# Optimization experiments

Measured on AMD Instinct MI355X. Metric: run time of the kernel, lower is better.

Reference implementation:

```python
import jax, jax.numpy as jnp
import numpy as np

N, E, D, H = 100000, 1000000, 64, 4
HD = D // H  # head dim
G = 64       # num graphs in batch
EPS = 1e-5
NEG_SLOPE = 0.2


def setup_inputs() -> dict:
    key = jax.random.key(0)
    ks = jax.random.split(key, 10)
    x = jax.random.normal(ks[0], (N, D), dtype=jnp.float32)
    edge_index = jax.random.randint(ks[1], (2, E), 0, N)
    batch = jnp.sort(jax.random.randint(ks[2], (N,), 0, G))
    s = 1.0 / np.sqrt(D)
    Wl = jax.random.uniform(ks[3], (D, D), jnp.float32, -s, s)   # lin_l (source)
    Wr = jax.random.uniform(ks[4], (D, D), jnp.float32, -s, s)   # lin_r (target)
    att = jax.random.uniform(ks[5], (H, HD), jnp.float32, -s, s)
    bias_gat = jnp.zeros((D,), jnp.float32)
    gn_weight = jnp.ones((D,), jnp.float32)
    gn_bias = jnp.zeros((D,), jnp.float32)
    gn_mean_scale = jnp.ones((D,), jnp.float32)
    return {"x": x, "edge_index": edge_index, "batch": batch, "Wl": Wl,
            "Wr": Wr, "att": att, "bias_gat": bias_gat, "gn_weight": gn_weight,
            "gn_bias": gn_bias, "gn_mean_scale": gn_mean_scale}


def _gatv2(x, src, dst, Wl, Wr, att, bias_gat):
    # per-node linear projections, reshaped to heads
    xl = (x @ Wl).reshape(N, H, HD)  # source features
    xr = (x @ Wr).reshape(N, H, HD)  # target features
    # per-edge attention logits: a^T LeakyReLU(xl_j + xr_i)
    e = xl[src] + xr[dst]                             # [E', H, HD]
    e = jnp.where(e >= 0, e, NEG_SLOPE * e)           # leaky_relu
    score = jnp.einsum('ehd,hd->eh', e, att)          # [E', H]
    # segment softmax over incoming edges of each dst node
    m = jax.ops.segment_max(score, dst, num_segments=N)   # [N, H]
    p = jnp.exp(score - m[dst])
    denom = jax.ops.segment_sum(p, dst, num_segments=N)   # [N, H]
    alpha = p / denom[dst]                                # [E', H]
    # weighted scatter-add aggregation of source features
    out = jax.ops.segment_sum(alpha[:, :, None] * xl[src], dst, num_segments=N)
    return out.reshape(N, D) + bias_gat


def _graph_norm(h, batch, weight, bias, mean_scale):
    cnt = jax.ops.segment_sum(jnp.ones((N,), h.dtype), batch, num_segments=G)
    cnt = jnp.maximum(cnt, 1.0)[:, None]                      # [G,1]
    mean = jax.ops.segment_sum(h, batch, num_segments=G) / cnt
    out = h - mean_scale * mean[batch]
    var = jax.ops.segment_sum(out * out, batch, num_segments=G) / cnt
    return weight * out / jnp.sqrt(var[batch] + EPS) + bias


def reference(x, edge_index, batch, Wl, Wr, att, bias_gat, gn_weight, gn_bias, gn_mean_scale):
    # eval mode: dropout / DropEdge are identity; pre_norm=False; res_proj=Identity
    loops = jnp.arange(N)
    src = jnp.concatenate([edge_index[0], loops])  # add self-loops (PyG default)
    dst = jnp.concatenate([edge_index[1], loops])
    h = _gatv2(x, src, dst, Wl, Wr, att, bias_gat)
    h = h + x                                       # identity residual
    h = jnp.where(h > 0, h, jnp.expm1(h))           # ELU
    h = _graph_norm(h, batch, gn_weight, gn_bias, gn_mean_scale)
    return h
```

## Files before the change

### kernel.cpp

```cpp
#include <hip/hip_runtime.h>
#include <hip/hip_bf16.h>
#include <math.h>

#define G_ 64
#define NEG_SLOPE 0.2f
#define EPS_ 1e-5f
#define BBITS 7
#define BSZ 128
#define CAP 2048
#define EPB 4096

typedef __attribute__((ext_vector_type(8))) unsigned short ushort8;
typedef __attribute__((ext_vector_type(8))) short bf16x8;
typedef __attribute__((ext_vector_type(4))) float f32x4;

#define DPP_ADD(t, ctrl)                                                   \
  do {                                                                     \
    int _p = __builtin_amdgcn_update_dpp(0, __float_as_int(t), (ctrl),     \
                                         0xf, 0xf, true);                  \
    (t) += __int_as_float(_p);                                             \
  } while (0)
#define REDUCE16(t)                                                        \
  do {                                                                     \
    DPP_ADD(t, 0xB1);                                                      \
    DPP_ADD(t, 0x4E);                                                      \
    DPP_ADD(t, 0x141);                                                     \
    DPP_ADD(t, 0x140);                                                     \
  } while (0)

__device__ __forceinline__ float leaky_(float e) {
  return 0.6f * e + 0.4f * fabsf(e);
}

__device__ __forceinline__ short f2bf(float f) {
  __hip_bfloat16 h = __float2bfloat16(f);
  return *reinterpret_cast<short*>(&h);
}

__global__ __launch_bounds__(256) void proj_mfma_kernel(
    const float* __restrict__ x, const float* __restrict__ Wl,
    const float* __restrict__ Wr, __hip_bfloat16* __restrict__ xlb,
    __hip_bfloat16* __restrict__ xrb, int n) {
  const int lane = threadIdx.x & 63;
  const int wv = threadIdx.x >> 6;
  const int rbase = blockIdx.x * 64 + wv * 16;
  const int lrow = lane & 15;
  const int lgrp = lane >> 4;

  bf16x8 bfrag[8][2];
#pragma unroll
  for (int ct = 0; ct < 8; ++ct) {
    const float* W = (ct < 4) ? Wl : Wr;
    const int col = ((ct & 3) * 16) + lrow;
#pragma unroll
    for (int kk = 0; kk < 2; ++kk) {
      const int kb = kk * 32 + lgrp * 8;
      bf16x8 f;
#pragma unroll
      for (int j = 0; j < 8; ++j) f[j] = f2bf(W[(kb + j) * 64 + col]);
      bfrag[ct][kk] = f;
    }
  }

  bf16x8 afrag[2];
  const int r = rbase + lrow;
#pragma unroll
  for (int kk = 0; kk < 2; ++kk) {
    bf16x8 f;
    if (r < n) {
      const float4* p = (const float4*)(x + (size_t)r * 64 + kk * 32 + lgrp * 8);
      float4 u = p[0], v = p[1];
      f[0] = f2bf(u.x); f[1] = f2bf(u.y); f[2] = f2bf(u.z); f[3] = f2bf(u.w);
      f[4] = f2bf(v.x); f[5] = f2bf(v.y); f[6] = f2bf(v.z); f[7] = f2bf(v.w);
    } else {
      f = bf16x8{0, 0, 0, 0, 0, 0, 0, 0};
    }
    afrag[kk] = f;
  }

  f32x4 acc[8];
#pragma unroll
  for (int ct = 0; ct < 8; ++ct) acc[ct] = f32x4{0.f, 0.f, 0.f, 0.f};
#pragma unroll
  for (int ct = 0; ct < 8; ++ct)
#pragma unroll
    for (int kk = 0; kk < 2; ++kk)
      acc[ct] = __builtin_amdgcn_mfma_f32_16x16x32_bf16(
          afrag[kk], bfrag[ct][kk], acc[ct], 0, 0, 0);

#pragma unroll
  for (int ct = 0; ct < 8; ++ct) {
    __hip_bfloat16* dst = (ct < 4) ? xlb : xrb;
    const int c = ((ct & 3) * 16) + lrow;
#pragma unroll
    for (int j = 0; j < 4; ++j) {
      const int rr = rbase + lgrp * 4 + j;
      if (rr < n) dst[(size_t)rr * 64 + c] = __float2bfloat16(acc[ct][j]);
    }
  }
}

__global__ __launch_bounds__(256) void bucket_kernel(
    const int* __restrict__ esrc, const int* __restrict__ edst,
    int* __restrict__ bcnt, unsigned int* __restrict__ packed,
    int e, int nb) {
  __shared__ int cnt[800];
  __shared__ int base[800];
  const int t = threadIdx.x;
  const int e0 = blockIdx.x * EPB;
  const int e1 = (e0 + EPB) < e ? (e0 + EPB) : e;
  for (int b = t; b < nb; b += 256) cnt[b] = 0;
  __syncthreads();
  for (int i = e0 + t; i < e1; i += 256)
    atomicAdd(&cnt[edst[i] >> BBITS], 1);
  __syncthreads();
  for (int b = t; b < nb; b += 256) {
    int c = cnt[b];
    base[b] = c ? atomicAdd(&bcnt[b], c) : 0;
    cnt[b] = 0;
  }
  __syncthreads();
  for (int i = e0 + t; i < e1; i += 256) {
    int d = edst[i];
    int b = d >> BBITS;
    int pos = base[b] + atomicAdd(&cnt[b], 1);
    if (pos < CAP)
      packed[(size_t)b * CAP + pos] =
          ((unsigned)(d & (BSZ - 1)) << 17) | (unsigned)esrc[i];
  }
}

__global__ __launch_bounds__(256) void sort_kernel(
    unsigned int* __restrict__ packed, const int* __restrict__ bcnt,
    int2* __restrict__ nse, int n) {
  __shared__ unsigned int stage[CAP];
  __shared__ int cnt[BSZ];
  __shared__ int sc[BSZ];
  __shared__ int off[BSZ + 1];
  const int t = threadIdx.x;
  const int b = blockIdx.x;
  int ecnt = bcnt[b];
  if (ecnt > CAP) ecnt = CAP;
  for (int j = t; j < ecnt; j += 256) stage[j] = packed[(size_t)b * CAP + j];
  if (t < BSZ) cnt[t] = 0;
  __syncthreads();
  for (int j = t; j < ecnt; j += 256) atomicAdd(&cnt[stage[j] >> 17], 1);
  __syncthreads();
  if (t < BSZ) sc[t] = cnt[t];
  __syncthreads();
#pragma unroll
  for (int o = 1; o < BSZ; o <<= 1) {
    int v = 0;
    if (t < BSZ && t >= o) v = sc[t - o];
    __syncthreads();
    if (t < BSZ) sc[t] += v;
    __syncthreads();
  }
  if (t < BSZ) {
    off[t + 1] = sc[t];
    if (t == 0) off[0] = 0;
    cnt[t] = sc[t] - cnt[t];
  }
  __syncthreads();
  for (int j = t; j < ecnt; j += 256) {
    unsigned v = stage[j];
    int pos = atomicAdd(&cnt[v >> 17], 1);
    packed[(size_t)b * CAP + pos] = v & 0x1FFFF;
  }
  const int nodebase = b << BBITS;
  if (t < BSZ && nodebase + t < n) {
    int s = off[t];
    nse[nodebase + t] = make_int2(b * CAP + s, off[t + 1] - s);
  }
}

__global__ __launch_bounds__(256) void aggregate_kernel(
    const __hip_bfloat16* __restrict__ xlb,
    const __hip_bfloat16* __restrict__ xrb, const float* __restrict__ x,
    const float* __restrict__ att, const float* __restrict__ bias_gat,
    const int2* __restrict__ nse, const unsigned int* __restrict__ srt,
    __hip_bfloat16* __restrict__ hb, int n) {
  const int lane = threadIdx.x & 63;
  const int i = (blockIdx.x * blockDim.x + threadIdx.x) >> 6;
  if (i >= n) return;
  const float attv = att[lane];
  const size_t rowoff = (size_t)i * 64 + lane;
  const float xrv = __bfloat162float(xrb[rowoff]);
  const float xlv = __bfloat162float(xlb[rowoff]);
  float t0 = leaky_(xlv + xrv) * attv;
  REDUCE16(t0);
  float p0 = __expf(t0);
  float acc = p0 * xlv;
  float den = p0;
  int2 sd = nse[i];
  const int s0 = __builtin_amdgcn_readfirstlane(sd.x);
  const int deg = __builtin_amdgcn_readfirstlane(sd.y);
  int myedge = (lane < deg) ? (int)srt[s0 + lane] : 0;
  const int kmax = deg < 64 ? deg : 64;
  int k = 0;
  for (; k + 3 < kmax; k += 4) {
    int sa = __builtin_amdgcn_readlane(myedge, k);
    int sb = __builtin_amdgcn_readlane(myedge, k + 1);
    int sc = __builtin_amdgcn_readlane(myedge, k + 2);
    int sdl = __builtin_amdgcn_readlane(myedge, k + 3);
    float xa = __bfloat162float(xlb[(size_t)sa * 64 + lane]);
    float xb = __bfloat162float(xlb[(size_t)sb * 64 + lane]);
    float xc = __bfloat162float(xlb[(size_t)sc * 64 + lane]);
    float xd = __bfloat162float(xlb[(size_t)sdl * 64 + lane]);
    float ta = leaky_(xa + xrv) * attv;
    float tb = leaky_(xb + xrv) * attv;
    float tc = leaky_(xc + xrv) * attv;
    float td = leaky_(xd + xrv) * attv;
    DPP_ADD(ta, 0xB1); DPP_ADD(tb, 0xB1); DPP_ADD(tc, 0xB1); DPP_ADD(td, 0xB1);
    DPP_ADD(ta, 0x4E); DPP_ADD(tb, 0x4E); DPP_ADD(tc, 0x4E); DPP_ADD(td, 0x4E);
    DPP_ADD(ta, 0x141); DPP_ADD(tb, 0x141); DPP_ADD(tc, 0x141); DPP_ADD(td, 0x141);
    DPP_ADD(ta, 0x140); DPP_ADD(tb, 0x140); DPP_ADD(tc, 0x140); DPP_ADD(td, 0x140);
    float pa = __expf(ta), pb = __expf(tb), pc = __expf(tc), pd = __expf(td);
    acc += pa * xa + pb * xb;
    acc += pc * xc + pd * xd;
    den += (pa + pb) + (pc + pd);
  }
  for (; k < kmax; ++k) {
    int s = __builtin_amdgcn_readlane(myedge, k);
    float xs = __bfloat162float(xlb[(size_t)s * 64 + lane]);
    float tt = leaky_(xs + xrv) * attv;
    REDUCE16(tt);
    float pp = __expf(tt);
    acc += pp * xs;
    den += pp;
  }
  for (int kk = 64; kk < deg; ++kk) {
    int s = (int)srt[s0 + kk];
    float xs = __bfloat162float(xlb[(size_t)s * 64 + lane]);
    float tt = leaky_(xs + xrv) * attv;
    REDUCE16(tt);
    float pp = __expf(tt);
    acc += pp * xs;
    den += pp;
  }
  float hv = acc / den + bias_gat[lane] + x[rowoff];
  hv = hv > 0.f ? hv : expm1f(hv);
  hb[rowoff] = __float2bfloat16(hv);
}

__global__ __launch_bounds__(256) void gsum2_kernel(
    const __hip_bfloat16* __restrict__ h, const int* __restrict__ batch,
    float* __restrict__ gsum, float* __restrict__ gsq,
    float* __restrict__ gcnt, int n) {
  const int lane = threadIdx.x & 63;
  const int wave = (blockIdx.x * blockDim.x + threadIdx.x) >> 6;
  const int nwaves = (gridDim.x * blockDim.x) >> 6;
  const int chunk = (n + nwaves - 1) / nwaves;
  const int start = wave * chunk;
  const int end = (start + chunk) < n ? (start + chunk) : n;
  float s1 = 0.f, s2 = 0.f, cntl = 0.f;
  int curg = -1;
  for (int i = start; i < end; ++i) {
    int g = batch[i];
    if (g != curg) {
      if (curg >= 0) {
        atomicAdd(&gsum[curg * 64 + lane], s1);
        atomicAdd(&gsq[curg * 64 + lane], s2);
        if (lane == 0) atomicAdd(&gcnt[curg], cntl);
      }
      curg = g; s1 = 0.f; s2 = 0.f; cntl = 0.f;
    }
    float hv = __bfloat162float(h[(size_t)i * 64 + lane]);
    s1 += hv;
    s2 += hv * hv;
    cntl += 1.f;
  }
  if (curg >= 0) {
    atomicAdd(&gsum[curg * 64 + lane], s1);
    atomicAdd(&gsq[curg * 64 + lane], s2);
    if (lane == 0) atomicAdd(&gcnt[curg], cntl);
  }
}

__global__ void stats_kernel(const float* __restrict__ gsum,
                             const float* __restrict__ gsq,
                             const float* __restrict__ gcnt,
                             const float* __restrict__ mscale,
                             const float* __restrict__ w,
                             float* __restrict__ msmean,
                             float* __restrict__ scale) {
  int i = blockIdx.x * blockDim.x + threadIdx.x;
  if (i < G_ * 64) {
    int dd = i & 63;
    float c = gcnt[i >> 6];
    c = c > 1.f ? c : 1.f;
    float mean = gsum[i] / c;
    float ms = mscale[dd];
    float var = gsq[i] / c - ms * (2.f - ms) * mean * mean;
    msmean[i] = ms * mean;
    scale[i] = w[dd] * rsqrtf(var + EPS_);
  }
}

__global__ __launch_bounds__(256) void out_kernel(
    const __hip_bfloat16* __restrict__ hb, const int* __restrict__ batch,
    const float* __restrict__ msmean, const float* __restrict__ scale,
    const float* __restrict__ bias, float* __restrict__ out, int n) {
  const int total8 = n * 8;
  for (int idx = blockIdx.x * blockDim.x + threadIdx.x; idx < total8;
       idx += gridDim.x * blockDim.x) {
    int i = idx >> 3, q = idx & 7;
    int g = batch[i];
    int base = g * 64 + q * 8;
    ushort8 hv8 = ((const ushort8*)hb)[idx];
    float r[8];
#pragma unroll
    for (int j = 0; j < 8; ++j) {
      float f = __uint_as_float(((unsigned)hv8[j]) << 16);
      r[j] = (f - msmean[base + j]) * scale[base + j] + bias[q * 8 + j];
    }
    float4 o0 = make_float4(r[0], r[1], r[2], r[3]);
    float4 o1 = make_float4(r[4], r[5], r[6], r[7]);
    ((float4*)out)[idx * 2] = o0;
    ((float4*)out)[idx * 2 + 1] = o1;
  }
}

extern "C" void kernel_launch(void* const* d_in, const int* in_sizes, int n_in,
                              void* d_out, int out_size, void* d_ws, size_t ws_size,
                              hipStream_t stream) {
  const float* x        = (const float*)d_in[0];
  const int*   eidx     = (const int*)d_in[1];
  const int*   batch    = (const int*)d_in[2];
  const float* Wl       = (const float*)d_in[3];
  const float* Wr       = (const float*)d_in[4];
  const float* att      = (const float*)d_in[5];
  const float* bias_gat = (const float*)d_in[6];
  const float* gw       = (const float*)d_in[7];
  const float* gb       = (const float*)d_in[8];
  const float* gms      = (const float*)d_in[9];
  const int N = in_sizes[0] / 64;
  const int E = in_sizes[1] / 2;
  const int* esrc = eidx;
  const int* edst = eidx + E;
  float* out = (float*)d_out;
  const int NB = (N + BSZ - 1) >> BBITS;

  char* wsp = (char*)d_ws;
  float* gsum   = (float*)wsp;                wsp += G_ * 64 * 4;
  float* gsq    = (float*)wsp;                wsp += G_ * 64 * 4;
  float* gcnt   = (float*)wsp;                wsp += G_ * 4;
  float* msmean = (float*)wsp;                wsp += G_ * 64 * 4;
  float* scale  = (float*)wsp;                wsp += G_ * 64 * 4;
  int*   bcnt   = (int*)wsp;                  wsp += (size_t)NB * 4;
  int2*  nse    = (int2*)wsp;                 wsp += (size_t)N * 8;
  unsigned int* packed = (unsigned int*)wsp;  wsp += (size_t)NB * CAP * 4;
  __hip_bfloat16* xlb = (__hip_bfloat16*)wsp; wsp += (size_t)N * 64 * 2;
  __hip_bfloat16* xrb = (__hip_bfloat16*)wsp; wsp += (size_t)N * 64 * 2;
  __hip_bfloat16* hb  = (__hip_bfloat16*)wsp; wsp += (size_t)N * 64 * 2;

  hipMemsetAsync(gsum, 0, (size_t)(2 * G_ * 64 + G_) * sizeof(float), stream);
  hipMemsetAsync(bcnt, 0, (size_t)NB * sizeof(int), stream);

  proj_mfma_kernel<<<(N + 63) / 64, 256, 0, stream>>>(x, Wl, Wr, xlb, xrb, N);

  const int ab = (E + EPB - 1) / EPB;
  bucket_kernel<<<ab, 256, 0, stream>>>(esrc, edst, bcnt, packed, E, NB);
  sort_kernel<<<NB, 256, 0, stream>>>(packed, bcnt, nse, N);

  aggregate_kernel<<<(N + 3) / 4, 256, 0, stream>>>(
      xlb, xrb, x, att, bias_gat, nse, packed, hb, N);

  gsum2_kernel<<<1024, 256, 0, stream>>>(hb, batch, gsum, gsq, gcnt, N);
  stats_kernel<<<(G_ * 64 + 255) / 256, 256, 0, stream>>>(gsum, gsq, gcnt, gms,
                                                          gw, msmean, scale);
  out_kernel<<<3125, 256, 0, stream>>>(hb, batch, msmean, scale, gb, out, N);
}
```

Baseline: 166.6 us.

## Process two edges per wave with half-wave lanes handling packed bf16 pairs

New measurement: 178.4 us. 7.1% more time.

```diff
diff --git a/kernel.cpp b/kernel.cpp
--- a/kernel.cpp
+++ b/kernel.cpp
@@ -8,7 +8,7 @@
 #define BBITS 7
 #define BSZ 128
 #define CAP 2048
-#define EPB 4096
+#define EPB 2048
 
 typedef __attribute__((ext_vector_type(8))) unsigned short ushort8;
 typedef __attribute__((ext_vector_type(8))) short bf16x8;
@@ -20,12 +20,11 @@
                                          0xf, 0xf, true);                  \
     (t) += __int_as_float(_p);                                             \
   } while (0)
-#define REDUCE16(t)                                                        \
+#define REDUCE8(t)                                                         \
   do {                                                                     \
     DPP_ADD(t, 0xB1);                                                      \
     DPP_ADD(t, 0x4E);                                                      \
     DPP_ADD(t, 0x141);                                                     \
-    DPP_ADD(t, 0x140);                                                     \
   } while (0)
 
 __device__ __forceinline__ float leaky_(float e) {
@@ -183,64 +182,75 @@
   const int lane = threadIdx.x & 63;
   const int i = (blockIdx.x * blockDim.x + threadIdx.x) >> 6;
   if (i >= n) return;
-  const float attv = att[lane];
-  const size_t rowoff = (size_t)i * 64 + lane;
-  const float xrv = __bfloat162float(xrb[rowoff]);
-  const float xlv = __bfloat162float(xlb[rowoff]);
-  float t0 = leaky_(xlv + xrv) * attv;
-  REDUCE16(t0);
-  float p0 = __expf(t0);
-  float acc = p0 * xlv;
-  float den = p0;
+  const int pos = lane & 31;
+  const int half = lane >> 5;
+  const float2 attp = ((const float2*)att)[pos];
+  const float a0 = attp.x * 1.44269504f;
+  const float a1 = attp.y * 1.44269504f;
+  const unsigned xr_pk = ((const unsigned*)(xrb + (size_t)i * 64))[pos];
+  const float xr0 = __uint_as_float(xr_pk << 16);
+  const float xr1 = __uint_as_float(xr_pk & 0xFFFF0000u);
   int2 sd = nse[i];
   const int s0 = __builtin_amdgcn_readfirstlane(sd.x);
   const int deg = __builtin_amdgcn_readfirstlane(sd.y);
-  int myedge = (lane < deg) ? (int)srt[s0 + lane] : 0;
-  const int kmax = deg < 64 ? deg : 64;
-  int k = 0;
-  for (; k + 3 < kmax; k += 4) {
-    int sa = __builtin_amdgcn_readlane(myedge, k);
-    int sb = __builtin_amdgcn_readlane(myedge, k + 1);
-    int sc = __builtin_amdgcn_readlane(myedge, k + 2);
-    int sdl = __builtin_amdgcn_readlane(myedge, k + 3);
-    float xa = __bfloat162float(xlb[(size_t)sa * 64 + lane]);
-    float xb = __bfloat162float(xlb[(size_t)sb * 64 + lane]);
-    float xc = __bfloat162float(xlb[(size_t)sc * 64 + lane]);
-    float xd = __bfloat162float(xlb[(size_t)sdl * 64 + lane]);
-    float ta = leaky_(xa + xrv) * attv;
-    float tb = leaky_(xb + xrv) * attv;
-    float tc = leaky_(xc + xrv) * attv;
-    float td = leaky_(xd + xrv) * attv;
-    DPP_ADD(ta, 0xB1); DPP_ADD(tb, 0xB1); DPP_ADD(tc, 0xB1); DPP_ADD(td, 0xB1);
-    DPP_ADD(ta, 0x4E); DPP_ADD(tb, 0x4E); DPP_ADD(tc, 0x4E); DPP_ADD(td, 0x4E);
-    DPP_ADD(ta, 0x141); DPP_ADD(tb, 0x141); DPP_ADD(tc, 0x141); DPP_ADD(td, 0x141);
-    DPP_ADD(ta, 0x140); DPP_ADD(tb, 0x140); DPP_ADD(tc, 0x140); DPP_ADD(td, 0x140);
-    float pa = __expf(ta), pb = __expf(tb), pc = __expf(tc), pd = __expf(td);
-    acc += pa * xa + pb * xb;
-    acc += pc * xc + pd * xd;
-    den += (pa + pb) + (pc + pd);
-  }
-  for (; k < kmax; ++k) {
-    int s = __builtin_amdgcn_readlane(myedge, k);
-    float xs = __bfloat162float(xlb[(size_t)s * 64 + lane]);
-    float tt = leaky_(xs + xrv) * attv;
-    REDUCE16(tt);
-    float pp = __expf(tt);
-    acc += pp * xs;
-    den += pp;
-  }
-  for (int kk = 64; kk < deg; ++kk) {
-    int s = (int)srt[s0 + kk];
-    float xs = __bfloat162float(xlb[(size_t)s * 64 + lane]);
-    float tt = leaky_(xs + xrv) * attv;
-    REDUCE16(tt);
-    float pp = __expf(tt);
-    acc += pp * xs;
-    den += pp;
-  }
-  float hv = acc / den + bias_gat[lane] + x[rowoff];
-  hv = hv > 0.f ? hv : expm1f(hv);
-  hb[rowoff] = __float2bfloat16(hv);
+  const int tot = deg + 1;
+  int myedge = i;
+  if (lane > 0 && lane < tot) myedge = (int)srt[s0 + lane - 1];
+  const int kmax = tot < 64 ? tot : 64;
+  float acc0 = 0.f, acc1 = 0.f, den = 0.f;
+  for (int k = 0; k < kmax; k += 2) {
+    const int sa = __builtin_amdgcn_readlane(myedge, k);
+    const int sb = (k + 1 < kmax) ? __builtin_amdgcn_readlane(myedge, k + 1)
+                                  : sa;
+    const int s = half ? sb : sa;
+    const unsigned byteoff = ((unsigned)s << 7) | ((unsigned)pos << 2);
+    const unsigned v =
+        *(const unsigned*)((const char*)xlb + byteoff);
+    const float l0 = __uint_as_float(v << 16);
+    const float l1 = __uint_as_float(v & 0xFFFF0000u);
+    float e0 = leaky_(l0 + xr0);
+    float e1 = leaky_(l1 + xr1);
+    float t = a0 * e0 + a1 * e1;
+    REDUCE8(t);
+    float p = exp2f(t);
+    p = ((k + half) < kmax) ? p : 0.f;
+    acc0 = fmaf(p, l0, acc0);
+    acc1 = fmaf(p, l1, acc1);
+    den += p;
+  }
+  for (int kk = 64; kk < tot; ++kk) {
+    const int s = (int)srt[s0 + kk - 1];
+    const unsigned byteoff = ((unsigned)s << 7) | ((unsigned)pos << 2);
+    const unsigned v = *(const unsigned*)((const char*)xlb + byteoff);
+    const float l0 = __uint_as_float(v << 16);
+    const float l1 = __uint_as_float(v & 0xFFFF0000u);
+    float e0 = leaky_(l0 + xr0);
+    float e1 = leaky_(l1 + xr1);
+    float t = a0 * e0 + a1 * e1;
+    REDUCE8(t);
+    float p = exp2f(t);
+    p = half ? 0.f : p;
+    acc0 = fmaf(p, l0, acc0);
+    acc1 = fmaf(p, l1, acc1);
+    den += p;
+  }
+  acc0 += __shfl_xor(acc0, 32);
+  acc1 += __shfl_xor(acc1, 32);
+  den += __shfl_xor(den, 32);
+  if (half == 0) {
+    const float inv = 1.f / den;
+    const float2 xres = ((const float2*)(x + (size_t)i * 64))[pos];
+    const float2 bb = ((const float2*)bias_gat)[pos];
+    float h0 = fmaf(acc0, inv, bb.x) + xres.x;
+    float h1 = fmaf(acc1, inv, bb.y) + xres.y;
+    h0 = h0 > 0.f ? h0 : expm1f(h0);
+    h1 = h1 > 0.f ? h1 : expm1f(h1);
+    __hip_bfloat16 b0 = __float2bfloat16(h0);
+    __hip_bfloat16 b1 = __float2bfloat16(h1);
+    unsigned pk = ((unsigned)(*(unsigned short*)&b1) << 16) |
+                  (unsigned)(*(unsigned short*)&b0);
+    ((unsigned*)(hb + (size_t)i * 64))[pos] = pk;
+  }
 }
 
 __global__ __launch_bounds__(256) void gsum2_kernel(
```
